# Kernel optimization log

Measured on AMD Instinct MI355X. Metric: run time of the kernel, lower is better.

The kernel has to match this reference:

```python
import jax, jax.numpy as jnp
import numpy as np

B, S, D, H, DH = 4, 2048, 1024, 16, 64  # batch, seq, d_model, heads, head_dim


def setup_inputs() -> dict:
    key = jax.random.key(0)
    ks = jax.random.split(key, 5)
    sc_in = 1.0 / np.sqrt(D)
    return {
        "x": jax.random.normal(ks[0], (B, S, D), dtype=jnp.float32),
        "Wq": jax.random.normal(ks[1], (H, D, DH), dtype=jnp.float32) * sc_in,
        "Wk": jax.random.normal(ks[2], (H, D, DH), dtype=jnp.float32) * sc_in,
        "Wv": jax.random.normal(ks[3], (H, D, DH), dtype=jnp.float32) * sc_in,
        "Wo": jax.random.normal(ks[4], (D, D), dtype=jnp.float32) * sc_in,
        "bo": jnp.zeros((D,), dtype=jnp.float32),
    }


def reference(x, Wq, Wk, Wv, Wo, bo):
    # Per-head Q/K/V projections (all heads batched in one einsum each).
    q = jnp.einsum("bsd,hde->bhse", x, Wq)  # [B,H,S,DH]
    k = jnp.einsum("bsd,hde->bhse", x, Wk)
    v = jnp.einsum("bsd,hde->bhse", x, Wv)
    scale = 1.0 / jnp.sqrt(jnp.asarray(DH, dtype=x.dtype))
    scores = jnp.einsum("bhse,bhte->bhst", q, k) * scale  # [B,H,S,S]
    causal = jnp.tril(jnp.ones((S, S), dtype=bool))
    scores = jnp.where(causal, scores, jnp.asarray(-jnp.inf, dtype=scores.dtype))
    attn = jax.nn.softmax(scores, axis=-1)
    heads = jnp.einsum("bhst,bhte->bhse", attn, v)  # [B,H,S,DH]
    # Concat heads (head-major order matches torch.cat of per-head outputs).
    concat = heads.transpose(0, 2, 1, 3).reshape(B, S, D)
    out = jnp.einsum("bsd,df->bsf", concat, Wo) + bo
    return out  # dropout_rate = 0.0 -> identity
```

## Files before the change

### kernel.cpp

```cpp
#include <hip/hip_runtime.h>
#include <hip/hip_bf16.h>

typedef __attribute__((ext_vector_type(8))) short short8;
typedef __attribute__((ext_vector_type(4))) float floatx4;

__device__ __forceinline__ short f2bf(float f) {
    unsigned u = __float_as_uint(f);
    u = u + 0x7fffu + ((u >> 16) & 1u);
    return (short)(u >> 16);
}
__device__ __forceinline__ short f2bf_rz(float f) {
    return (short)(__float_as_uint(f) >> 16);
}

static constexpr int B_ = 4, S_ = 2048, D_ = 1024, H_ = 16, DH_ = 64;
static constexpr float QSCALE = 0.125f * 1.4426950408889634f;

__global__ __launch_bounds__(256) void convert_x(const float* __restrict__ in,
                                                 short* __restrict__ out, int n8) {
    int i = blockIdx.x * 256 + threadIdx.x;
    if (i >= n8) return;
    const float4* p = (const float4*)(in + (size_t)i * 8);
    float4 a = p[0], b = p[1];
    short8 v;
    v[0] = f2bf(a.x); v[1] = f2bf(a.y); v[2] = f2bf(a.z); v[3] = f2bf(a.w);
    v[4] = f2bf(b.x); v[5] = f2bf(b.y); v[6] = f2bf(b.z); v[7] = f2bf(b.w);
    *(short8*)(out + (size_t)i * 8) = v;
}

__global__ __launch_bounds__(256) void prep_weights(const float* __restrict__ Wq,
                                                    const float* __restrict__ Wk,
                                                    const float* __restrict__ Wv,
                                                    const float* __restrict__ Wo,
                                                    short* __restrict__ WqT,
                                                    short* __restrict__ WkT,
                                                    short* __restrict__ WvT,
                                                    short* __restrict__ WoT) {
    __shared__ alignas(16) float t[64 * 68];
    int z = blockIdx.z;
    const float* in;
    short* out;
    int N, M = D_, n0;
    if (z < 3) {
        const float* I = (z == 0) ? Wq : (z == 1) ? Wk : Wv;
        short* O = (z == 0) ? WqT : (z == 1) ? WkT : WvT;
        in = I + (size_t)blockIdx.y * D_ * DH_;
        out = O + (size_t)blockIdx.y * D_ * DH_;
        N = DH_; n0 = 0;
    } else {
        in = Wo; out = WoT; N = D_; n0 = blockIdx.y * 64;
    }
    int m0 = blockIdx.x * 64;
    int tid = threadIdx.x;
#pragma unroll
    for (int i = 0; i < 4; ++i) {
        int c = tid + i * 256;
        int row = c >> 4, c4 = (c & 15) * 4;
        float4 v = *(const float4*)(in + (size_t)(m0 + row) * N + n0 + c4);
        *(float4*)(t + row * 68 + c4) = v;
    }
    __syncthreads();
#pragma unroll
    for (int i = 0; i < 2; ++i) {
        int c = tid + i * 256;
        int row = c >> 3, c8 = (c & 7) * 8;
        short8 v;
#pragma unroll
        for (int j = 0; j < 8; ++j) v[j] = f2bf(t[(c8 + j) * 68 + row]);
        *(short8*)(out + (size_t)(n0 + row) * M + m0 + c8) = v;
    }
}

__device__ __forceinline__ void gemm128_core(const short* __restrict__ A,
                                             const short* __restrict__ Bm,
                                             short* ldsA, short* ldsB,
                                             int m0, int n0,
                                             floatx4 (&acc)[4][4],
                                             int w, int lane, int quad, int lm) {
    const int K = 1024;
    int wm = (w >> 1) * 64, wn = (w & 1) * 64;
    int rsub = lane >> 3;
    int csw = ((lane & 7) ^ rsub) * 8;
    int lmx = lm & 7;
    for (int k0 = 0; k0 < K; k0 += 64) {
#pragma unroll
        for (int i = 0; i < 4; ++i) {
            int r0 = w * 32 + i * 8;
            const short* ga = A + (size_t)(m0 + r0 + rsub) * K + k0 + csw;
            __builtin_amdgcn_global_load_lds((const __attribute__((address_space(1))) void*)ga,
                                             (__attribute__((address_space(3))) void*)(ldsA + r0 * 64),
                                             16, 0, 0);
            const short* gb = Bm + (size_t)(n0 + r0 + rsub) * K + k0 + csw;
            __builtin_amdgcn_global_load_lds((const __attribute__((address_space(1))) void*)gb,
                                             (__attribute__((address_space(3))) void*)(ldsB + r0 * 64),
                                             16, 0, 0);
        }
        __syncthreads();
#pragma unroll
        for (int ks = 0; ks < 2; ++ks) {
            short8 am[4], bn[4];
#pragma unroll
            for (int i = 0; i < 4; ++i)
                am[i] = *(const short8*)(ldsA + (wm + i * 16 + lm) * 64 + (((ks * 4 + quad) ^ lmx) << 3));
#pragma unroll
            for (int i = 0; i < 4; ++i)
                bn[i] = *(const short8*)(ldsB + (wn + i * 16 + lm) * 64 + (((ks * 4 + quad) ^ lmx) << 3));
#pragma unroll
            for (int mi = 0; mi < 4; ++mi)
#pragma unroll
                for (int ni = 0; ni < 4; ++ni)
                    acc[mi][ni] = __builtin_amdgcn_mfma_f32_16x16x32_bf16(am[mi], bn[ni], acc[mi][ni], 0, 0, 0);
        }
        __syncthreads();
    }
}

__global__ __launch_bounds__(256, 4) void qkv_gemm128(const short* __restrict__ xb,
                                                      const short* __restrict__ WqT,
                                                      const short* __restrict__ WkT,
                                                      const short* __restrict__ WvT,
                                                      short* __restrict__ Q,
                                                      short* __restrict__ K,
                                                      short* __restrict__ VT) {
    __shared__ alignas(16) short lds[16384];
    short* ldsA = lds;
    short* ldsB = lds + 8192;
    int m0 = blockIdx.x * 128, n0 = blockIdx.y * 128, z = blockIdx.z;
    const short* Bm = (z == 0) ? WqT : (z == 1) ? WkT : WvT;
    int tid = threadIdx.x, w = tid >> 6, lane = tid & 63, quad = lane >> 4, lm = lane & 15;

    floatx4 acc[4][4];
#pragma unroll
    for (int mi = 0; mi < 4; ++mi)
#pragma unroll
        for (int ni = 0; ni < 4; ++ni) acc[mi][ni] = (floatx4)0.0f;

    gemm128_core(xb, Bm, ldsA, ldsB, m0, n0, acc, w, lane, quad, lm);

    int wm = (w >> 1) * 64, wn = (w & 1) * 64;
    int b = m0 >> 11;
    int sbase = m0 & 2047;

    if (z < 2) {
        short* O = (z == 0) ? Q : K;
        float scale = (z == 0) ? QSCALE : 1.0f;
        short* t = lds;
#pragma unroll
        for (int ph = 0; ph < 2; ++ph) {
            if (ph) __syncthreads();
            if ((w & 1) == ph) {
#pragma unroll
                for (int mi = 0; mi < 4; ++mi)
#pragma unroll
                    for (int ni = 0; ni < 4; ++ni)
#pragma unroll
                        for (int r = 0; r < 4; ++r)
                            t[(wm + mi * 16 + quad * 4 + r) * 68 + ni * 16 + lm] =
                                f2bf(acc[mi][ni][r] * scale);
            }
            __syncthreads();
            int h = (n0 + ph * 64) >> 6;
            size_t obase = ((size_t)(b * 16 + h) * 2048 + sbase) * 64;
#pragma unroll
            for (int i = 0; i < 4; ++i) {
                int c = tid + i * 256;
                int m = c >> 3, e8 = (c & 7) * 8;
                short8 v = *(const short8*)(t + m * 68 + e8);
                *(short8*)(O + obase + (size_t)m * 64 + e8) = v;
            }
        }
    } else {
        short* t = lds;
#pragma unroll
        for (int ph = 0; ph < 2; ++ph) {
            if (ph) __syncthreads();
            if ((w & 1) == ph) {
#pragma unroll
                for (int mi = 0; mi < 4; ++mi)
#pragma unroll
                    for (int ni = 0; ni < 4; ++ni) {
                        int nl = ni * 16 + lm;
#pragma unroll
                        for (int r = 0; r < 4; ++r) {
                            int ml = wm + mi * 16 + quad * 4 + r;
                            t[nl * 136 + ml] = f2bf(acc[mi][ni][r]);
                        }
                    }
            }
            __syncthreads();
#pragma unroll
            for (int i = 0; i < 4; ++i) {
                int c = tid + i * 256;
                int rowl = c >> 4, colc = (c & 15) * 8;
                short8 v = *(const short8*)(t + rowl * 136 + colc);
                size_t n = n0 + ph * 64 + rowl;
                *(short8*)(VT + ((size_t)b * 1024 + n) * 2048 + sbase + colc) = v;
            }
        }
    }
}

__global__ __launch_bounds__(256, 4) void outproj128(const short* __restrict__ CC,
                                                     const short* __restrict__ WoT,
                                                     const float* __restrict__ bo,
                                                     float* __restrict__ out) {
    __shared__ alignas(16) short lds[16384];
    short* ldsA = lds;
    short* ldsB = lds + 8192;
    int m0 = blockIdx.x * 128, n0 = blockIdx.y * 128;
    int tid = threadIdx.x, w = tid >> 6, lane = tid & 63, quad = lane >> 4, lm = lane & 15;

    floatx4 acc[4][4];
#pragma unroll
    for (int mi = 0; mi < 4; ++mi)
#pragma unroll
        for (int ni = 0; ni < 4; ++ni) acc[mi][ni] = (floatx4)0.0f;

    gemm128_core(CC, WoT, ldsA, ldsB, m0, n0, acc, w, lane, quad, lm);

    int wm = (w >> 1) * 64, wn = (w & 1) * 64;
#pragma unroll
    for (int mi = 0; mi < 4; ++mi)
#pragma unroll
        for (int ni = 0; ni < 4; ++ni) {
            int n = n0 + wn + ni * 16 + lm;
            float bb = bo[n];
#pragma unroll
            for (int r = 0; r < 4; ++r) {
                int m = m0 + wm + mi * 16 + quad * 4 + r;
                out[(size_t)m * 1024 + n] = acc[mi][ni][r] + bb;
            }
        }
}

__global__ __launch_bounds__(256) void attn_kernel(const short* __restrict__ Q,
                                                   const short* __restrict__ Kb,
                                                   const short* __restrict__ VT,
                                                   short* __restrict__ CC) {
    __shared__ alignas(16) short Kt[128 * 64];
    __shared__ alignas(16) short Vt[64 * 128];
    __shared__ alignas(16) short Pt[64 * 136];
    int pi = blockIdx.x;
    int bh = blockIdx.y;
    int b = bh >> 4, h = bh & 15;
    int tid = threadIdx.x;
    int w = tid >> 6, l = tid & 63;
    int quad = l >> 4, lm = l & 15;
    int lmx = lm & 7;
    int rsub = l >> 3;
    int csw = ((l & 7) ^ rsub) * 8;
    int vr4 = l >> 4;
    int vc = l & 15;

    const short* Qbh = Q + (size_t)bh * S_ * DH_;
    const short* Kbh = Kb + (size_t)bh * S_ * DH_;
    const short* Vbh = VT + (size_t)bh * 64 * S_;

    for (int ps = 0; ps < 2; ++ps) {
        int qt = ps ? (31 - pi) : pi;
        int q0 = qt * 64;

        const short* Qrow = Qbh + (size_t)(q0 + w * 16 + lm) * DH_;
        short8 qa0 = *(const short8*)(Qrow + quad * 8);
        short8 qa1 = *(const short8*)(Qrow + 32 + quad * 8);

        floatx4 acc_o[4];
#pragma unroll
        for (int ct = 0; ct < 4; ++ct) acc_o[ct] = (floatx4)0.0f;
        float lsum[4] = {0.0f, 0.0f, 0.0f, 0.0f};

        int nkt = (qt >> 1) + 1;
        for (int kt = 0; kt < nkt; ++kt) {
            int t0 = kt * 128;
            const short* Ktile = Kbh + (size_t)t0 * DH_;
#pragma unroll
            for (int i = 0; i < 4; ++i) {
                int r0 = w * 32 + i * 8;
                const short* ga = Ktile + (size_t)(r0 + rsub) * 64 + csw;
                __builtin_amdgcn_global_load_lds((const __attribute__((address_space(1))) void*)ga,
                                                 (__attribute__((address_space(3))) void*)(Kt + r0 * 64),
                                                 16, 0, 0);
            }
#pragma unroll
            for (int i = 0; i < 4; ++i) {
                int r0v = w * 16 + i * 4;
                int row = r0v + vr4;
                int key = row & 7;
                const short* gv = Vbh + (size_t)row * S_ + t0 + ((vc ^ key) * 8);
                __builtin_amdgcn_global_load_lds((const __attribute__((address_space(1))) void*)gv,
                                                 (__attribute__((address_space(3))) void*)(Vt + r0v * 128),
                                                 16, 0, 0);
            }
            __syncthreads();

            floatx4 sc[8];
#pragma unroll
            for (int ct = 0; ct < 8; ++ct) {
                const short* kr = Kt + (ct * 16 + lm) * 64;
                short8 k0 = *(const short8*)(kr + ((quad ^ lmx) << 3));
                short8 k1 = *(const short8*)(kr + (((4 + quad) ^ lmx) << 3));
                floatx4 t = (floatx4)0.0f;
                t = __builtin_amdgcn_mfma_f32_16x16x32_bf16(qa0, k0, t, 0, 0, 0);
                t = __builtin_amdgcn_mfma_f32_16x16x32_bf16(qa1, k1, t, 0, 0, 0);
                sc[ct] = t;
            }
            if (kt == nkt - 1) {
#pragma unroll
                for (int ct = 0; ct < 8; ++ct)
#pragma unroll
                    for (int r = 0; r < 4; ++r) {
                        int tcol = t0 + ct * 16 + lm;
                        int qrow = q0 + w * 16 + quad * 4 + r;
                        if (tcol > qrow) sc[ct][r] = -INFINITY;
                    }
            }
#pragma unroll
            for (int ct = 0; ct < 8; ++ct)
#pragma unroll
                for (int r = 0; r < 4; ++r) {
                    float p = exp2f(sc[ct][r]);
                    lsum[r] += p;
                    Pt[(w * 16 + quad * 4 + r) * 136 + ct * 16 + lm] = f2bf_rz(p);
                }
            short8 pa[4];
#pragma unroll
            for (int ks = 0; ks < 4; ++ks)
                pa[ks] = *(const short8*)(Pt + (w * 16 + lm) * 136 + ks * 32 + quad * 8);
#pragma unroll
            for (int ct = 0; ct < 4; ++ct) {
                const short* vrow = Vt + (ct * 16 + lm) * 128;
#pragma unroll
                for (int ks = 0; ks < 4; ++ks) {
                    short8 v = *(const short8*)(vrow + (((ks * 4 + quad) ^ lmx) << 3));
                    acc_o[ct] = __builtin_amdgcn_mfma_f32_16x16x32_bf16(pa[ks], v, acc_o[ct], 0, 0, 0);
                }
            }
            __syncthreads();
        }

        float inv[4];
#pragma unroll
        for (int r = 0; r < 4; ++r) {
            float lr = lsum[r];
#pragma unroll
            for (int off = 1; off < 16; off <<= 1) lr += __shfl_xor(lr, off);
            inv[r] = 1.0f / lr;
        }

        short* OC = CC + ((size_t)b * S_ + q0) * D_ + h * DH_;
#pragma unroll
        for (int ct = 0; ct < 4; ++ct)
#pragma unroll
            for (int r = 0; r < 4; ++r) {
                int row = w * 16 + quad * 4 + r;
                OC[(size_t)row * D_ + ct * 16 + lm] = f2bf(acc_o[ct][r] * inv[r]);
            }
    }
}

extern "C" void kernel_launch(void* const* d_in, const int* in_sizes, int n_in,
                              void* d_out, int out_size, void* d_ws, size_t ws_size,
                              hipStream_t stream) {
    const float* x  = (const float*)d_in[0];
    const float* Wq = (const float*)d_in[1];
    const float* Wk = (const float*)d_in[2];
    const float* Wv = (const float*)d_in[3];
    const float* Wo = (const float*)d_in[4];
    const float* bo = (const float*)d_in[5];
    float* out = (float*)d_out;
    short* ws = (short*)d_ws;

    const size_t WSZ = (size_t)H_ * D_ * DH_;
    const size_t QSZ = (size_t)B_ * H_ * S_ * DH_;
    short* WqT = ws;
    short* WkT = WqT + WSZ;
    short* WvT = WkT + WSZ;
    short* WoT = WvT + WSZ;
    short* xb  = WoT + (size_t)D_ * D_;
    short* Qb  = xb + (size_t)B_ * S_ * D_;
    short* Kb  = Qb + QSZ;
    short* VTb = Kb + QSZ;
    short* CCb = VTb + QSZ;

    convert_x<<<(B_ * S_ * D_ / 8 + 255) / 256, 256, 0, stream>>>(x, xb, B_ * S_ * D_ / 8);
    prep_weights<<<dim3(16, 16, 4), 256, 0, stream>>>(Wq, Wk, Wv, Wo, WqT, WkT, WvT, WoT);
    qkv_gemm128<<<dim3(64, 8, 3), 256, 0, stream>>>(xb, WqT, WkT, WvT, Qb, Kb, VTb);
    attn_kernel<<<dim3(16, B_ * H_), 256, 0, stream>>>(Qb, Kb, VTb, CCb);
    outproj128<<<dim3(64, 8), 256, 0, stream>>>(CCb, WoT, bo, out);
}
```

Baseline: 286.1 us.

## Process 128 query rows per attention block to reuse K/V tiles across two subtiles

The attention kernel now handles 128-row query tiles as two 64-row subtiles, so each K/V tile loaded into LDS serves twice as many queries. The score MFMA is transposed (K as the A operand) so P can be written to LDS as packed 4-element stores with an XOR swizzle. The row-sum reduction is adjusted to match. The grid halves to 8 blocks per head and launch_bounds requests 2 blocks per CU. This cuts global/LDS traffic per query but raises register pressure and halves block count, which may hurt occupancy and load balance.

```diff
diff --git a/kernel.cpp b/kernel.cpp
--- a/kernel.cpp
+++ b/kernel.cpp
@@ -2,6 +2,7 @@
 #include <hip/hip_bf16.h>
 
 typedef __attribute__((ext_vector_type(8))) short short8;
+typedef __attribute__((ext_vector_type(4))) short short4x;
 typedef __attribute__((ext_vector_type(4))) float floatx4;
 
 __device__ __forceinline__ short f2bf(float f) {
@@ -233,13 +234,13 @@
         }
 }
 
-__global__ __launch_bounds__(256) void attn_kernel(const short* __restrict__ Q,
-                                                   const short* __restrict__ Kb,
-                                                   const short* __restrict__ VT,
-                                                   short* __restrict__ CC) {
+__global__ __launch_bounds__(256, 2) void attn_kernel(const short* __restrict__ Q,
+                                                      const short* __restrict__ Kb,
+                                                      const short* __restrict__ VT,
+                                                      short* __restrict__ CC) {
     __shared__ alignas(16) short Kt[128 * 64];
     __shared__ alignas(16) short Vt[64 * 128];
-    __shared__ alignas(16) short Pt[64 * 136];
+    __shared__ alignas(16) short Pt[128 * 128];
     int pi = blockIdx.x;
     int bh = blockIdx.y;
     int b = bh >> 4, h = bh & 15;
@@ -257,19 +258,25 @@
     const short* Vbh = VT + (size_t)bh * 64 * S_;
 
     for (int ps = 0; ps < 2; ++ps) {
-        int qt = ps ? (31 - pi) : pi;
-        int q0 = qt * 64;
-
-        const short* Qrow = Qbh + (size_t)(q0 + w * 16 + lm) * DH_;
-        short8 qa0 = *(const short8*)(Qrow + quad * 8);
-        short8 qa1 = *(const short8*)(Qrow + 32 + quad * 8);
-
-        floatx4 acc_o[4];
-#pragma unroll
-        for (int ct = 0; ct < 4; ++ct) acc_o[ct] = (floatx4)0.0f;
-        float lsum[4] = {0.0f, 0.0f, 0.0f, 0.0f};
-
-        int nkt = (qt >> 1) + 1;
+        int qt = ps ? (15 - pi) : pi;
+        int q0 = qt * 128;
+
+        short8 qa[2][2];
+#pragma unroll
+        for (int nq = 0; nq < 2; ++nq) {
+            const short* Qrow = Qbh + (size_t)(q0 + nq * 64 + w * 16 + lm) * DH_;
+            qa[nq][0] = *(const short8*)(Qrow + quad * 8);
+            qa[nq][1] = *(const short8*)(Qrow + 32 + quad * 8);
+        }
+
+        floatx4 acc_o[2][4];
+#pragma unroll
+        for (int nq = 0; nq < 2; ++nq)
+#pragma unroll
+            for (int ct = 0; ct < 4; ++ct) acc_o[nq][ct] = (floatx4)0.0f;
+        float lsum[2] = {0.0f, 0.0f};
+
+        int nkt = qt + 1;
         for (int kt = 0; kt < nkt; ++kt) {
             int t0 = kt * 128;
             const short* Ktile = Kbh + (size_t)t0 * DH_;
@@ -285,76 +292,97 @@
             for (int i = 0; i < 4; ++i) {
                 int r0v = w * 16 + i * 4;
                 int row = r0v + vr4;
-                int key = row & 7;
-                const short* gv = Vbh + (size_t)row * S_ + t0 + ((vc ^ key) * 8);
+                const short* gv = Vbh + (size_t)row * S_ + t0 + ((vc ^ (row & 7)) * 8);
                 __builtin_amdgcn_global_load_lds((const __attribute__((address_space(1))) void*)gv,
                                                  (__attribute__((address_space(3))) void*)(Vt + r0v * 128),
                                                  16, 0, 0);
             }
             __syncthreads();
 
-            floatx4 sc[8];
-#pragma unroll
-            for (int ct = 0; ct < 8; ++ct) {
-                const short* kr = Kt + (ct * 16 + lm) * 64;
-                short8 k0 = *(const short8*)(kr + ((quad ^ lmx) << 3));
-                short8 k1 = *(const short8*)(kr + (((4 + quad) ^ lmx) << 3));
-                floatx4 t = (floatx4)0.0f;
-                t = __builtin_amdgcn_mfma_f32_16x16x32_bf16(qa0, k0, t, 0, 0, 0);
-                t = __builtin_amdgcn_mfma_f32_16x16x32_bf16(qa1, k1, t, 0, 0, 0);
-                sc[ct] = t;
-            }
-            if (kt == nkt - 1) {
-#pragma unroll
-                for (int ct = 0; ct < 8; ++ct)
-#pragma unroll
-                    for (int r = 0; r < 4; ++r) {
-                        int tcol = t0 + ct * 16 + lm;
-                        int qrow = q0 + w * 16 + quad * 4 + r;
-                        if (tcol > qrow) sc[ct][r] = -INFINITY;
-                    }
-            }
-#pragma unroll
-            for (int ct = 0; ct < 8; ++ct)
-#pragma unroll
-                for (int r = 0; r < 4; ++r) {
-                    float p = exp2f(sc[ct][r]);
-                    lsum[r] += p;
-                    Pt[(w * 16 + quad * 4 + r) * 136 + ct * 16 + lm] = f2bf_rz(p);
+            short8 kf[8][2];
+#pragma unroll
+            for (int mt = 0; mt < 8; ++mt)
+#pragma unroll
+                for (int ks = 0; ks < 2; ++ks)
+                    kf[mt][ks] = *(const short8*)(Kt + (mt * 16 + lm) * 64 + (((ks * 4 + quad) ^ lmx) << 3));
+
+            bool last = (kt == nkt - 1);
+#pragma unroll
+            for (int nq = 0; nq < 2; ++nq) {
+                floatx4 sc[8];
+#pragma unroll
+                for (int mt = 0; mt < 8; ++mt) {
+                    floatx4 t = (floatx4)0.0f;
+                    t = __builtin_amdgcn_mfma_f32_16x16x32_bf16(kf[mt][0], qa[nq][0], t, 0, 0, 0);
+                    t = __builtin_amdgcn_mfma_f32_16x16x32_bf16(kf[mt][1], qa[nq][1], t, 0, 0, 0);
+                    sc[mt] = t;
                 }
-            short8 pa[4];
-#pragma unroll
-            for (int ks = 0; ks < 4; ++ks)
-                pa[ks] = *(const short8*)(Pt + (w * 16 + lm) * 136 + ks * 32 + quad * 8);
+                if (last) {
+                    int q_ = q0 + nq * 64 + w * 16 + lm;
+#pragma unroll
+                    for (int mt = 0; mt < 8; ++mt)
+#pragma unroll
+                        for (int r = 0; r < 4; ++r) {
+                            int t_ = t0 + mt * 16 + quad * 4 + r;
+                            if (t_ > q_) sc[mt][r] = -INFINITY;
+                        }
+                }
+                int prow = nq * 64 + w * 16 + lm;
+#pragma unroll
+                for (int mt = 0; mt < 8; ++mt) {
+                    float p0 = exp2f(sc[mt][0]);
+                    float p1 = exp2f(sc[mt][1]);
+                    float p2 = exp2f(sc[mt][2]);
+                    float p3 = exp2f(sc[mt][3]);
+                    lsum[nq] += (p0 + p1) + (p2 + p3);
+                    short4x pk;
+                    pk[0] = f2bf_rz(p0); pk[1] = f2bf_rz(p1);
+                    pk[2] = f2bf_rz(p2); pk[3] = f2bf_rz(p3);
+                    int c = mt * 2 + (quad >> 1);
+                    *(short4x*)(Pt + prow * 128 + ((c ^ lmx) << 3) + (quad & 1) * 4) = pk;
+                }
+            }
+            short8 pa[2][4];
+#pragma unroll
+            for (int nq = 0; nq < 2; ++nq)
+#pragma unroll
+                for (int ks = 0; ks < 4; ++ks)
+                    pa[nq][ks] = *(const short8*)(Pt + (nq * 64 + w * 16 + lm) * 128 +
+                                                  (((ks * 4 + quad) ^ lmx) << 3));
 #pragma unroll
             for (int ct = 0; ct < 4; ++ct) {
                 const short* vrow = Vt + (ct * 16 + lm) * 128;
 #pragma unroll
                 for (int ks = 0; ks < 4; ++ks) {
                     short8 v = *(const short8*)(vrow + (((ks * 4 + quad) ^ lmx) << 3));
-                    acc_o[ct] = __builtin_amdgcn_mfma_f32_16x16x32_bf16(pa[ks], v, acc_o[ct], 0, 0, 0);
+                    acc_o[0][ct] = __builtin_amdgcn_mfma_f32_16x16x32_bf16(pa[0][ks], v, acc_o[0][ct], 0, 0, 0);
+                    acc_o[1][ct] = __builtin_amdgcn_mfma_f32_16x16x32_bf16(pa[1][ks], v, acc_o[1][ct], 0, 0, 0);
                 }
             }
             __syncthreads();
         }
 
-        float inv[4];
-#pragma unroll
-        for (int r = 0; r < 4; ++r) {
-            float lr = lsum[r];
-#pragma unroll
-            for (int off = 1; off < 16; off <<= 1) lr += __shfl_xor(lr, off);
-            inv[r] = 1.0f / lr;
-        }
-
-        short* OC = CC + ((size_t)b * S_ + q0) * D_ + h * DH_;
-#pragma unroll
-        for (int ct = 0; ct < 4; ++ct)
+        float invl[2];
+#pragma unroll
+        for (int nq = 0; nq < 2; ++nq) {
+            float lr = lsum[nq];
+            lr += __shfl_xor(lr, 16);
+            lr += __shfl_xor(lr, 32);
+            invl[nq] = 1.0f / lr;
+        }
+
+#pragma unroll
+        for (int nq = 0; nq < 2; ++nq) {
 #pragma unroll
             for (int r = 0; r < 4; ++r) {
-                int row = w * 16 + quad * 4 + r;
-                OC[(size_t)row * D_ + ct * 16 + lm] = f2bf(acc_o[ct][r] * inv[r]);
-            }
+                float iv = __shfl(invl[nq], quad * 4 + r);
+                int row = q0 + nq * 64 + w * 16 + quad * 4 + r;
+                short* OC = CC + ((size_t)b * S_ + row) * D_ + h * DH_;
+#pragma unroll
+                for (int ct = 0; ct < 4; ++ct)
+                    OC[ct * 16 + lm] = f2bf(acc_o[nq][ct][r] * iv);
+            }
+        }
     }
 }
 
@@ -385,6 +413,6 @@
     convert_x<<<(B_ * S_ * D_ / 8 + 255) / 256, 256, 0, stream>>>(x, xb, B_ * S_ * D_ / 8);
     prep_weights<<<dim3(16, 16, 4), 256, 0, stream>>>(Wq, Wk, Wv, Wo, WqT, WkT, WvT, WoT);
     qkv_gemm128<<<dim3(64, 8, 3), 256, 0, stream>>>(xb, WqT, WkT, WvT, Qb, Kb, VTb);
-    attn_kernel<<<dim3(16, B_ * H_), 256, 0, stream>>>(Qb, Kb, VTb, CCb);
+    attn_kernel<<<dim3(8, B_ * H_), 256, 0, stream>>>(Qb, Kb, VTb, CCb);
     outproj128<<<dim3(64, 8), 256, 0, stream>>>(CCb, WoT, bo, out);
 }
```

After: 240.4 us. 1.19x faster.
